# Performance work log

Hardware: AMD Instinct MI355X
Metric: run time of the kernel (lower is better)

Reference implementation:

```python
import jax, jax.numpy as jnp
import numpy as np

N_NODES = 20000
N_EDGES = 320000
N_GRAPHS = 64
IN_DIM = 768
HID = 256
HEADS = 4
NUM_CLASSES = 5
NEG_SLOPE = 0.2  # PyG GATConv default leaky_relu slope


def setup_inputs() -> dict:
    key = jax.random.key(0)
    ks = jax.random.split(key, 20)
    x = jax.random.normal(ks[0], (N_NODES, IN_DIM), dtype=jnp.float32)
    edge_index = jax.random.randint(ks[1], (2, N_EDGES), 0, N_NODES, dtype=jnp.int32)
    batch = jnp.sort(jax.random.randint(ks[2], (N_NODES,), 0, N_GRAPHS, dtype=jnp.int32))
    s = lambda k, sh: jax.random.normal(k, sh, dtype=jnp.float32) * (1.0 / np.sqrt(sh[0]))
    HC = HEADS * HID
    return {
        "x": x, "edge_index": edge_index, "batch": batch,
        "Wp": s(ks[3], (IN_DIM, HID)), "bp": jnp.zeros((HID,), jnp.float32),
        "W1": s(ks[4], (HID, HC)),
        "as1": jax.random.normal(ks[5], (HEADS, HID)) * 0.1,
        "ad1": jax.random.normal(ks[6], (HEADS, HID)) * 0.1,
        "b1": jnp.zeros((HC,), jnp.float32),
        "W2": s(ks[7], (HC, HC)),
        "as2": jax.random.normal(ks[8], (HEADS, HID)) * 0.1,
        "ad2": jax.random.normal(ks[9], (HEADS, HID)) * 0.1,
        "b2": jnp.zeros((HC,), jnp.float32),
        "Wc1": s(ks[10], (2 * HC, 256)), "bc1": jnp.zeros((256,), jnp.float32),
        "Wc2": s(ks[11], (256, NUM_CLASSES)), "bc2": jnp.zeros((NUM_CLASSES,), jnp.float32),
    }


def _gat(h, src, dst, W, att_s, att_d, bias):
    # PyG GATConv (concat=True), dropout in eval mode (identity).
    N = h.shape[0]
    hW = (h @ W).reshape(N, HEADS, HID)             # [N,H,C]
    a_s = jnp.einsum('nhc,hc->nh', hW, att_s)        # per-node src score
    a_d = jnp.einsum('nhc,hc->nh', hW, att_d)
    e = jax.nn.leaky_relu(a_s[src] + a_d[dst], NEG_SLOPE)  # [E,H]
    # segment softmax over incoming edges of each destination node
    m = jax.ops.segment_max(e, dst, num_segments=N)
    e = jnp.exp(e - m[dst])
    denom = jax.ops.segment_sum(e, dst, num_segments=N)
    alpha = e / (denom[dst] + 1e-16)
    msg = hW[src] * alpha[:, :, None]                # [E,H,C]
    out = jax.ops.segment_sum(msg, dst, num_segments=N)
    return out.reshape(N, HEADS * HID) + bias


def reference(x, edge_index, batch, Wp, bp, W1, as1, ad1, b1, W2, as2, ad2, b2, Wc1, bc1, Wc2, bc2):
    N = x.shape[0]
    # add self-loops (PyG GATConv default add_self_loops=True)
    loop = jnp.arange(N, dtype=edge_index.dtype)
    src = jnp.concatenate([edge_index[0], loop])
    dst = jnp.concatenate([edge_index[1], loop])

    h = jax.nn.relu(x @ Wp + bp)
    h = jax.nn.elu(_gat(h, src, dst, W1, as1, ad1, b1))
    h = jax.nn.elu(_gat(h, src, dst, W2, as2, ad2, b2))

    # global mean / max pool over graphs
    cnt = jax.ops.segment_sum(jnp.ones((N,), h.dtype), batch, num_segments=N_GRAPHS)
    mean_pool = jax.ops.segment_sum(h, batch, num_segments=N_GRAPHS) / jnp.maximum(cnt, 1.0)[:, None]
    max_pool = jax.ops.segment_max(h, batch, num_segments=N_GRAPHS)
    g = jnp.concatenate([mean_pool, max_pool], axis=1)  # [G, 2*H*C]

    hcls = jax.nn.relu(g @ Wc1 + bc1)
    return hcls @ Wc2 + bc2
```

## Files before the change

kernel.cpp:

```cpp
#include <hip/hip_runtime.h>
#include <hip/hip_fp16.h>
#include <math.h>

#define N_HID 256
#define N_HEADS 4
#define N_HC 1024
#define N_GRAPHS 64

typedef __attribute__((ext_vector_type(4))) float f32x4;
typedef _Float16 half8 __attribute__((ext_vector_type(8)));
typedef _Float16 half4 __attribute__((ext_vector_type(4)));

__device__ __forceinline__ void gl_lds16h(const __half* g, __half* l) {
    __builtin_amdgcn_global_load_lds(
        (const __attribute__((address_space(1))) unsigned int*)g,
        (__attribute__((address_space(3))) unsigned int*)l, 16, 0, 0);
}

__global__ __launch_bounds__(256) void k_deg(const int* __restrict__ dst, int E,
                                             int* __restrict__ deg) {
    int e = blockIdx.x * 256 + threadIdx.x;
    if (e < E) atomicAdd(&deg[dst[e]], 1);
}

__global__ __launch_bounds__(1024) void k_scan(const int* __restrict__ deg,
                                               int* __restrict__ rowstart, int N) {
    __shared__ int part[1024];
    const int t = threadIdx.x;
    const int chunk = (N + 1023) / 1024;
    const int c0 = t * chunk;
    int s = 0;
    for (int i = 0; i < chunk; i++) {
        int idx = c0 + i;
        if (idx < N) s += deg[idx];
    }
    part[t] = s;
    __syncthreads();
    for (int off = 1; off < 1024; off <<= 1) {
        int v = (t >= off) ? part[t - off] : 0;
        __syncthreads();
        part[t] += v;
        __syncthreads();
    }
    int run = (t == 0) ? 0 : part[t - 1];
    if (t == 0) rowstart[0] = 0;
    for (int i = 0; i < chunk; i++) {
        int idx = c0 + i;
        if (idx < N) {
            run += deg[idx];
            rowstart[idx + 1] = run;
        }
    }
}

__global__ __launch_bounds__(256) void k_fill(const int* __restrict__ src,
                                              const int* __restrict__ dst, int E,
                                              const int* __restrict__ rowstart,
                                              int* __restrict__ cursor,
                                              int* __restrict__ col) {
    int e = blockIdx.x * 256 + threadIdx.x;
    if (e < E) {
        int d = dst[e];
        int p = atomicAdd(&cursor[d], 1);
        col[rowstart[d] + p] = src[e];
    }
}

__global__ __launch_bounds__(256) void k_wtt(const float* __restrict__ W,
                                             __half* __restrict__ WT, int K, int N) {
    __shared__ float tile[32][33];
    const int k0 = blockIdx.y * 32, n0 = blockIdx.x * 32;
    const int tr = threadIdx.x >> 5, tc = threadIdx.x & 31;
#pragma unroll
    for (int rr = 0; rr < 4; rr++) {
        int k = k0 + tr + rr * 8;
        tile[tr + rr * 8][tc] = W[(size_t)k * N + n0 + tc];
    }
    __syncthreads();
#pragma unroll
    for (int rr = 0; rr < 4; rr++) {
        int n = n0 + tr + rr * 8;
        WT[(size_t)n * K + k0 + tc] = __float2half(tile[tc][tr + rr * 8]);
    }
}

__global__ __launch_bounds__(256) void k_makeva(const __half* __restrict__ W1T,
                                                const float* __restrict__ as1,
                                                const float* __restrict__ ad1,
                                                float* __restrict__ va) {
    __shared__ float satt[256];
    int b = blockIdx.x;
    int h = b & 3, isd = b >> 2;
    int k = threadIdx.x;
    const float* att = (isd ? ad1 : as1) + h * 256;
    satt[k] = att[k];
    __syncthreads();
    const __half* wr = W1T + (size_t)(h * 256) * 256 + k;
    float s = 0.f;
    for (int c = 0; c < 256; c++) s += __half2float(wr[(size_t)c * 256]) * satt[c];
    va[b * 256 + k] = s;
}

__global__ __launch_bounds__(256) void k_makeva2(const __half* __restrict__ W2T,
                                                 const float* __restrict__ as2,
                                                 const float* __restrict__ ad2,
                                                 float* __restrict__ va2) {
    __shared__ float satt[32];
    int b = blockIdx.x;
    int h = b & 3;
    int jc = blockIdx.y;
    int t = threadIdx.x;
    const float* att = (b >= 4 ? ad2 : as2) + h * 256 + jc * 32;
    if (t < 32) satt[t] = att[t];
    __syncthreads();
    float s0 = 0.f, s1 = 0.f, s2 = 0.f, s3 = 0.f;
    const __half* base = W2T + (size_t)(h * 256 + jc * 32) * 1024 + t * 4;
    for (int j = 0; j < 32; j++) {
        half4 wv = *reinterpret_cast<const half4*>(base + (size_t)j * 1024);
        float a = satt[j];
        s0 += a * (float)wv[0]; s1 += a * (float)wv[1];
        s2 += a * (float)wv[2]; s3 += a * (float)wv[3];
    }
    float* o = va2 + b * 1024 + t * 4;
    atomicAdd(o + 0, s0); atomicAdd(o + 1, s1);
    atomicAdd(o + 2, s2); atomicAdd(o + 3, s3);
}

template <int EPI, int COSCHED>
__global__ __launch_bounds__(256) void k_gemm2p(
    const __half* __restrict__ A, const __half* __restrict__ BT,
    const float* __restrict__ bias, __half* __restrict__ C,
    int M, int NROW, int K, int lda, int ldc,
    int aoffz, int boffz, int coffz, int bofz) {
    __shared__ __half sA[2][128 * 32];
    __shared__ __half sB[2][128 * 32];
    int bm, bn;
    size_t coff = 0;
    if (COSCHED) {
        const int bid = blockIdx.x;
        const int xcd = bid & 7, j0 = bid >> 3;
        const int br = xcd + 8 * (j0 >> 3);
        const int bc = j0 & 7;
        if (br >= NROW) return;
        bm = br * 128; bn = bc * 128;
    } else {
        const int z = blockIdx.z;
        A += (size_t)z * aoffz;
        BT += (size_t)z * boffz;
        bias += z * bofz;
        coff = (size_t)z * coffz;
        bm = blockIdx.y * 128; bn = blockIdx.x * 128;
    }
    const int tid = threadIdx.x, lane = tid & 63, w = tid >> 6;
    const int wr = (w >> 1) * 64, wc = (w & 1) * 64;
    const bool isB = (w >= 2);
    const __half* gsrc = isB ? (BT + (size_t)bn * K) : (A + (size_t)bm * lda);
    const int gld = isB ? K : lda;
    const int rbase = (w & 1) * 64;
    const int lr = lane >> 2, lsl = lane & 3;
    const int g = lane >> 4, fr = lane & 15;
    const int nt = K >> 5;

    f32x4 acc[4][4] = {};

    auto STAGE = [&](int b, int t) {
        __half* sbuf = (isB ? sB[b] : sA[b]);
        const int k0 = t << 5;
#pragma unroll
        for (int c2 = 0; c2 < 4; c2++) {
            int row = rbase + c2 * 16 + lr;
            int slg = lsl ^ ((row >> 1) & 3);
            gl_lds16h(gsrc + (size_t)row * gld + k0 + slg * 8,
                      sbuf + (rbase + c2 * 16) * 32);
        }
    };

    STAGE(0, 0);
    int cur = 0;
    for (int t = 0; t < nt; ++t) {
        if (t + 1 < nt) {
            STAGE(cur ^ 1, t + 1);
            asm volatile("s_waitcnt vmcnt(4)" ::: "memory");
        } else {
            asm volatile("s_waitcnt vmcnt(0)" ::: "memory");
        }
        asm volatile("s_barrier" ::: "memory");
        half8 af[4], bf[4];
#pragma unroll
        for (int i = 0; i < 4; i++) {
            int Ra = wr + i * 16 + fr;
            af[i] = *reinterpret_cast<const half8*>(
                &sA[cur][Ra * 32 + ((g ^ ((Ra >> 1) & 3)) << 3)]);
            int Rb = wc + i * 16 + fr;
            bf[i] = *reinterpret_cast<const half8*>(
                &sB[cur][Rb * 32 + ((g ^ ((Rb >> 1) & 3)) << 3)]);
        }
#pragma unroll
        for (int i = 0; i < 4; i++)
#pragma unroll
            for (int j = 0; j < 4; j++)
                acc[i][j] = __builtin_amdgcn_mfma_f32_16x16x32_f16(af[i], bf[j], acc[i][j], 0, 0, 0);
        asm volatile("s_barrier" ::: "memory");
        cur ^= 1;
    }
    const int crow0 = (lane >> 4) * 4, ccol = lane & 15;
#pragma unroll
    for (int i = 0; i < 4; i++)
#pragma unroll
        for (int j = 0; j < 4; j++) {
            int cc = bn + wc + j * 16 + ccol;
            float bv = (EPI == 2) ? bias[cc] : 0.f;
#pragma unroll
            for (int r = 0; r < 4; r++) {
                int row = bm + wr + i * 16 + crow0 + r;
                if (row < M) {
                    float v = acc[i][j][r];
                    if (EPI == 2) { v += bv; v = v > 0.f ? v : (__expf(v) - 1.f); }
                    C[(size_t)row * ldc + coff + cc] = __float2half(v);
                }
            }
        }
}

__global__ __launch_bounds__(256) void k_gemm_x(
    const float* __restrict__ A, const __half* __restrict__ BT,
    const float* __restrict__ bias, __half* __restrict__ C,
    int M, int NROW, int K, int lda) {
    __shared__ __half sA[128 * 32];
    __shared__ __half sB[128 * 32];
    const int bid = blockIdx.x;
    const int xcd = bid & 7, j0 = bid >> 3;
    const int br = xcd + 8 * (j0 >> 1);
    const int bc = j0 & 1;
    if (br >= NROW) return;
    const int bm = br * 128, bn = bc * 128;
    const int tid = threadIdx.x, lane = tid & 63, w = tid >> 6;
    const int wr = (w >> 1) * 64, wc = (w & 1) * 64;
    const int sm = tid >> 1, skb = (tid & 1) * 16;
    const bool rok = (bm + sm) < M;
    const int ph0 = (((tid & 1) * 2 + 0) ^ ((sm >> 1) & 3)) << 3;
    const int ph1 = (((tid & 1) * 2 + 1) ^ ((sm >> 1) & 3)) << 3;
    const int lr = lane >> 2, lsl = lane & 3;

    f32x4 acc[4][4] = {};

    for (int k0 = 0; k0 < K; k0 += 32) {
#pragma unroll
        for (int c = 0; c < 2; c++) {
            int rb = (w + c * 4) * 16;
            int row = rb + lr;
            int slg = lsl ^ ((row >> 1) & 3);
            gl_lds16h(BT + (size_t)(bn + row) * K + k0 + slg * 8, sB + rb * 32);
        }
        {
            const float* Arow = A + (size_t)(bm + sm) * lda + k0 + skb;
            float4 v0 = make_float4(0.f, 0.f, 0.f, 0.f), v1 = v0, v2 = v0, v3 = v0;
            if (rok) {
                v0 = *(const float4*)(Arow + 0);
                v1 = *(const float4*)(Arow + 4);
                v2 = *(const float4*)(Arow + 8);
                v3 = *(const float4*)(Arow + 12);
            }
            half8 ha, hb;
            ha[0] = (_Float16)v0.x; ha[1] = (_Float16)v0.y;
            ha[2] = (_Float16)v0.z; ha[3] = (_Float16)v0.w;
            ha[4] = (_Float16)v1.x; ha[5] = (_Float16)v1.y;
            ha[6] = (_Float16)v1.z; ha[7] = (_Float16)v1.w;
            hb[0] = (_Float16)v2.x; hb[1] = (_Float16)v2.y;
            hb[2] = (_Float16)v2.z; hb[3] = (_Float16)v2.w;
            hb[4] = (_Float16)v3.x; hb[5] = (_Float16)v3.y;
            hb[6] = (_Float16)v3.z; hb[7] = (_Float16)v3.w;
            *reinterpret_cast<half8*>(&sA[sm * 32 + ph0]) = ha;
            *reinterpret_cast<half8*>(&sA[sm * 32 + ph1]) = hb;
        }
        __syncthreads();
        half8 af[4], bf[4];
        const int g = lane >> 4, fr = lane & 15;
#pragma unroll
        for (int i = 0; i < 4; i++) {
            int Ra = wr + i * 16 + fr;
            af[i] = *reinterpret_cast<const half8*>(
                &sA[Ra * 32 + ((g ^ ((Ra >> 1) & 3)) << 3)]);
            int Rb = wc + i * 16 + fr;
            bf[i] = *reinterpret_cast<const half8*>(
                &sB[Rb * 32 + ((g ^ ((Rb >> 1) & 3)) << 3)]);
        }
#pragma unroll
        for (int i = 0; i < 4; i++)
#pragma unroll
            for (int j = 0; j < 4; j++)
                acc[i][j] = __builtin_amdgcn_mfma_f32_16x16x32_f16(af[i], bf[j], acc[i][j], 0, 0, 0);
        __syncthreads();
    }
    const int crow0 = (lane >> 4) * 4, ccol = lane & 15;
#pragma unroll
    for (int i = 0; i < 4; i++)
#pragma unroll
        for (int j = 0; j < 4; j++) {
            int cc = bn + wc + j * 16 + ccol;
            float bv = bias[cc];
#pragma unroll
            for (int r = 0; r < 4; r++) {
                int row = bm + wr + i * 16 + crow0 + r;
                if (row < M) {
                    float v = acc[i][j][r] + bv;
                    v = v > 0.f ? v : 0.f;
                    C[(size_t)row * 256 + cc] = __float2half(v);
                }
            }
        }
}

__global__ __launch_bounds__(256) void k_score8(const __half* __restrict__ h0,
                                                const float* __restrict__ va,
                                                float* __restrict__ a_s,
                                                float* __restrict__ a_d, int N) {
    __shared__ float sva[8][256];
    int t = threadIdx.x;
    for (int i = t; i < 2048; i += 256) sva[i >> 8][i & 255] = va[i];
    __syncthreads();
    int wv = t >> 6, lane = t & 63;
    int n = blockIdx.x * 4 + wv;
    if (n >= N) return;
    uint2 u = *(const uint2*)(h0 + (size_t)n * 256 + lane * 4);
    __half2 q0 = __builtin_bit_cast(__half2, u.x);
    __half2 q1 = __builtin_bit_cast(__half2, u.y);
    float v0 = __half2float(q0.x), v1 = __half2float(q0.y);
    float v2 = __half2float(q1.x), v3 = __half2float(q1.y);
    float p[8];
#pragma unroll
    for (int v = 0; v < 8; v++) {
        p[v] = v0 * sva[v][lane * 4] + v1 * sva[v][lane * 4 + 1] +
               v2 * sva[v][lane * 4 + 2] + v3 * sva[v][lane * 4 + 3];
    }
#pragma unroll
    for (int off = 32; off > 0; off >>= 1)
#pragma unroll
        for (int v = 0; v < 8; v++) p[v] += __shfl_xor(p[v], off, 64);
    if (lane == 0) {
        *(float4*)&a_s[n * 4] = make_float4(p[0], p[1], p[2], p[3]);
        *(float4*)&a_d[n * 4] = make_float4(p[4], p[5], p[6], p[7]);
    }
}

__global__ __launch_bounds__(256) void k_score1024(const __half* __restrict__ h1,
                                                   const float* __restrict__ va2,
                                                   float* __restrict__ a_s,
                                                   float* __restrict__ a_d, int N) {
    __shared__ float sva[8 * 1024];
    int t = threadIdx.x;
    for (int i = t; i < 8192; i += 256) sva[i] = va2[i];
    __syncthreads();
    int wv = t >> 6, lane = t & 63;
    int n = blockIdx.x * 4 + wv;
    if (n >= N) return;
    const __half* hp = h1 + (size_t)n * 1024;
    float hv[16];
#pragma unroll
    for (int seg = 0; seg < 4; seg++) {
        half4 u = *reinterpret_cast<const half4*>(hp + seg * 256 + lane * 4);
#pragma unroll
        for (int c = 0; c < 4; c++) hv[seg * 4 + c] = (float)u[c];
    }
    float p[8] = {};
#pragma unroll
    for (int v = 0; v < 8; v++) {
#pragma unroll
        for (int seg = 0; seg < 4; seg++) {
            float4 f = *(const float4*)&sva[v * 1024 + seg * 256 + lane * 4];
            p[v] += hv[seg * 4] * f.x + hv[seg * 4 + 1] * f.y +
                    hv[seg * 4 + 2] * f.z + hv[seg * 4 + 3] * f.w;
        }
    }
#pragma unroll
    for (int off = 32; off > 0; off >>= 1)
#pragma unroll
        for (int v = 0; v < 8; v++) p[v] += __shfl_xor(p[v], off, 64);
    if (lane == 0) {
        *(float4*)&a_s[n * 4] = make_float4(p[0], p[1], p[2], p[3]);
        *(float4*)&a_d[n * 4] = make_float4(p[4], p[5], p[6], p[7]);
    }
}

__global__ __launch_bounds__(256) void k_alpha(
    const float* __restrict__ a_s, const float* __restrict__ a_d,
    const int* __restrict__ rowstart, const int* __restrict__ col,
    __half* __restrict__ alp, float* __restrict__ invS, int N) {
    const int w = threadIdx.x >> 6, lane = threadIdx.x & 63;
    const int n = blockIdx.x * 4 + w;
    if (n >= N) return;
    const int e0 = rowstart[n];
    const int deg = rowstart[n + 1] - e0;
    const int tot = deg + 1;
    const int as0 = e0 + n;
    float4 adv4 = *(const float4*)&a_d[n * 4];
    const float adv[4] = {adv4.x, adv4.y, adv4.z, adv4.w};
    float M[4] = {-INFINITY, -INFINITY, -INFINITY, -INFINITY};
    for (int base = 0; base < tot; base += 64) {
        const int li = base + lane;
        float e[4] = {-INFINITY, -INFINITY, -INFINITY, -INFINITY};
        if (li < tot) {
            const int sn = (li < deg) ? col[e0 + li] : n;
            float4 asv = *(const float4*)&a_s[sn * 4];
            const float as4[4] = {asv.x, asv.y, asv.z, asv.w};
#pragma unroll
            for (int h = 0; h < 4; h++) {
                float sc = as4[h] + adv[h];
                e[h] = sc >= 0.f ? sc : 0.2f * sc;
            }
        }
#pragma unroll
        for (int off = 32; off > 0; off >>= 1)
#pragma unroll
            for (int h = 0; h < 4; h++)
                e[h] = fmaxf(e[h], __shfl_xor(e[h], off, 64));
#pragma unroll
        for (int h = 0; h < 4; h++) M[h] = fmaxf(M[h], e[h]);
    }
    float S[4] = {0.f, 0.f, 0.f, 0.f};
    for (int base = 0; base < tot; base += 64) {
        const int li = base + lane;
        float wv[4] = {0.f, 0.f, 0.f, 0.f};
        if (li < tot) {
            const int sn = (li < deg) ? col[e0 + li] : n;
            float4 asv = *(const float4*)&a_s[sn * 4];
            const float as4[4] = {asv.x, asv.y, asv.z, asv.w};
            half4 o;
#pragma unroll
            for (int h = 0; h < 4; h++) {
                float sc = as4[h] + adv[h];
                float e = sc >= 0.f ? sc : 0.2f * sc;
                wv[h] = __expf(e - M[h]);
                o[h] = (_Float16)wv[h];
            }
            *reinterpret_cast<half4*>(alp + (size_t)(as0 + li) * 4) = o;
        }
        float sw[4] = {wv[0], wv[1], wv[2], wv[3]};
#pragma unroll
        for (int off = 32; off > 0; off >>= 1)
#pragma unroll
            for (int h = 0; h < 4; h++) sw[h] += __shfl_xor(sw[h], off, 64);
#pragma unroll
        for (int h = 0; h < 4; h++) S[h] += sw[h];
    }
    if (lane == 0) {
        *(float4*)&invS[n * 4] = make_float4(
            1.f / (S[0] + 1e-16f), 1.f / (S[1] + 1e-16f),
            1.f / (S[2] + 1e-16f), 1.f / (S[3] + 1e-16f));
    }
}

__global__ __launch_bounds__(256) void k_gath1(
    const __half* __restrict__ h0, const __half* __restrict__ alp,
    const float* __restrict__ invS, const int* __restrict__ rowstart,
    const int* __restrict__ col, __half* __restrict__ agg1, int N) {
    __shared__ int wsn[4][64];
    __shared__ float wal[4][64][4];
    const int w = threadIdx.x >> 6, lane = threadIdx.x & 63;
    const int bid = blockIdx.x;
    const int s = bid & 1;
    const int n = (bid >> 1) * 4 + w;
    if (n >= N) return;
    const int e0 = rowstart[n];
    const int deg = rowstart[n + 1] - e0;
    const int tot = deg + 1;
    const int as0 = e0 + n;
    float acc[4][2] = {};

    for (int base = 0; base < tot; base += 64) {
        const int cnt = min(64, tot - base);
        const int li = base + lane;
        if (li < tot) {
            wsn[w][lane] = (li < deg) ? col[e0 + li] : n;
            half4 av = *reinterpret_cast<const half4*>(alp + (size_t)(as0 + li) * 4);
            *(float4*)&wal[w][lane][0] = make_float4(
                (float)av[0], (float)av[1], (float)av[2], (float)av[3]);
        }
        const __half* gbase = h0 + s * 128 + lane * 2;
#pragma unroll 2
        for (int i = 0; i < cnt; i++) {
            const int s2 = wsn[w][i];
            float4 wg = *(const float4*)&wal[w][i][0];
            const float wgt[4] = {wg.x, wg.y, wg.z, wg.w};
            __half2 hv = *(const __half2*)(gbase + (size_t)s2 * 256);
            float v0 = __half2float(hv.x), v1 = __half2float(hv.y);
#pragma unroll
            for (int h = 0; h < 4; h++) {
                acc[h][0] += wgt[h] * v0;
                acc[h][1] += wgt[h] * v1;
            }
        }
    }
    float4 dv = *(const float4*)&invS[n * 4];
    const float d[4] = {dv.x, dv.y, dv.z, dv.w};
#pragma unroll
    for (int h = 0; h < 4; h++) {
        __half2 o;
        o.x = __float2half(acc[h][0] * d[h]);
        o.y = __float2half(acc[h][1] * d[h]);
        *(__half2*)(agg1 + (size_t)n * 1024 + h * 256 + s * 128 + lane * 2) = o;
    }
}

__global__ __launch_bounds__(256) void k_gath2(
    const __half* __restrict__ hW, const __half* __restrict__ alp,
    const float* __restrict__ invS, const int* __restrict__ rowstart,
    const int* __restrict__ col, const float* __restrict__ bias,
    __half* __restrict__ h2, int N) {
    __shared__ int wsn[4][64];
    __shared__ float wal[4][64];
    const int w = threadIdx.x >> 6, lane = threadIdx.x & 63;
    const int bid = blockIdx.x;
    const int h = bid & 3;
    const int n = (bid >> 2) * 4 + w;
    if (n >= N) return;
    const int e0 = rowstart[n];
    const int deg = rowstart[n + 1] - e0;
    const int tot = deg + 1;
    const int as0 = e0 + n;
    float acc[4] = {};

    for (int base = 0; base < tot; base += 64) {
        const int cnt = min(64, tot - base);
        const int li = base + lane;
        if (li < tot) {
            wsn[w][lane] = (li < deg) ? col[e0 + li] : n;
            wal[w][lane] = (float)alp[(size_t)(as0 + li) * 4 + h];
        }
        const __half* gbase = hW + h * 256 + lane * 4;
#pragma unroll 4
        for (int i = 0; i < cnt; i++) {
            const int s2 = wsn[w][i];
            const float a = wal[w][i];
            half4 v = *reinterpret_cast<const half4*>(gbase + (size_t)s2 * 1024);
#pragma unroll
            for (int c = 0; c < 4; c++) acc[c] += a * (float)v[c];
        }
    }
    const float d = invS[n * 4 + h];
    const int cc = h * 256 + lane * 4;
    float4 bb = *(const float4*)&bias[cc];
    const float bv[4] = {bb.x, bb.y, bb.z, bb.w};
    half4 o;
#pragma unroll
    for (int c = 0; c < 4; c++) {
        float v = acc[c] * d + bv[c];
        v = v > 0.f ? v : (__expf(v) - 1.f);
        o[c] = (_Float16)v;
    }
    *reinterpret_cast<half4*>(h2 + (size_t)n * 1024 + cc) = o;
}

__global__ __launch_bounds__(128) void k_gbounds(const int* __restrict__ batch, int N,
                                                 int* __restrict__ gstart) {
    int g = threadIdx.x;
    if (g > N_GRAPHS) return;
    if (g == N_GRAPHS) { gstart[N_GRAPHS] = N; return; }
    int lo = 0, hi = N;
    while (lo < hi) {
        int mid = (lo + hi) >> 1;
        if (batch[mid] < g) lo = mid + 1; else hi = mid;
    }
    gstart[g] = lo;
}

__global__ __launch_bounds__(256) void k_pool1(const __half* __restrict__ h,
                                               const int* __restrict__ gstart,
                                               float* __restrict__ ps) {
    const int g = blockIdx.x, c = blockIdx.y, t = threadIdx.x;
    const int s = gstart[g], e = gstart[g + 1];
    const int len = e - s;
    const int cs = s + (int)(((long long)len * c) >> 3);
    const int ce = s + (int)(((long long)len * (c + 1)) >> 3);
    float sum[4] = {};
    float mx[4] = {-INFINITY, -INFINITY, -INFINITY, -INFINITY};
    for (int i = cs; i < ce; i++) {
        half4 v = *reinterpret_cast<const half4*>(h + (size_t)i * N_HC + t * 4);
#pragma unroll
        for (int k = 0; k < 4; k++) {
            float f = (float)v[k];
            sum[k] += f;
            mx[k] = fmaxf(mx[k], f);
        }
    }
    float* o = ps + ((size_t)g * 8 + c) * 2048;
    *(float4*)&o[t * 4] = make_float4(sum[0], sum[1], sum[2], sum[3]);
    *(float4*)&o[1024 + t * 4] = make_float4(mx[0], mx[1], mx[2], mx[3]);
}

__global__ __launch_bounds__(256) void k_pool2(const float* __restrict__ ps,
                                               const int* __restrict__ gstart,
                                               float* __restrict__ gout) {
    const int g = blockIdx.x, t = threadIdx.x;
    float sum[4] = {};
    float mx[4] = {-INFINITY, -INFINITY, -INFINITY, -INFINITY};
#pragma unroll
    for (int c = 0; c < 8; c++) {
        const float* o = ps + ((size_t)g * 8 + c) * 2048;
        float4 sv = *(const float4*)&o[t * 4];
        float4 mv = *(const float4*)&o[1024 + t * 4];
        sum[0] += sv.x; sum[1] += sv.y; sum[2] += sv.z; sum[3] += sv.w;
        mx[0] = fmaxf(mx[0], mv.x); mx[1] = fmaxf(mx[1], mv.y);
        mx[2] = fmaxf(mx[2], mv.z); mx[3] = fmaxf(mx[3], mv.w);
    }
    float cnt = fmaxf((float)(gstart[g + 1] - gstart[g]), 1.f);
    float inv = 1.f / cnt;
    *(float4*)(gout + (size_t)g * 2048 + t * 4) =
        make_float4(sum[0] * inv, sum[1] * inv, sum[2] * inv, sum[3] * inv);
    *(float4*)(gout + (size_t)g * 2048 + 1024 + t * 4) =
        make_float4(mx[0], mx[1], mx[2], mx[3]);
}

__global__ __launch_bounds__(256) void k_cls1p(const float* __restrict__ g,
                                               const float* __restrict__ Wc1,
                                               float* __restrict__ hacc) {
    __shared__ float gs[256];
    const int gb = blockIdx.x, kc = blockIdx.y, t = threadIdx.x;
    gs[t] = g[(size_t)gb * 2048 + kc * 256 + t];
    __syncthreads();
    float acc = 0.f;
    const float* wb = Wc1 + (size_t)(kc * 256) * 256 + t;
#pragma unroll 4
    for (int k = 0; k < 256; k++) acc += gs[k] * wb[(size_t)k * 256];
    atomicAdd(&hacc[gb * 256 + t], acc);
}

__global__ __launch_bounds__(256) void k_cls2(const float* __restrict__ hacc,
                                              const float* __restrict__ bc1,
                                              const float* __restrict__ Wc2,
                                              const float* __restrict__ bc2,
                                              float* __restrict__ out) {
    int idx = blockIdx.x * 256 + threadIdx.x;
    if (idx >= N_GRAPHS * 5) return;
    int gb = idx / 5, j = idx % 5;
    float acc = 0.f;
    for (int k = 0; k < 256; k++) {
        float v = hacc[gb * 256 + k] + bc1[k];
        v = v > 0.f ? v : 0.f;
        acc += v * Wc2[k * 5 + j];
    }
    out[idx] = acc + bc2[j];
}

extern "C" void kernel_launch(void* const* d_in, const int* in_sizes, int n_in,
                              void* d_out, int out_size, void* d_ws, size_t ws_size,
                              hipStream_t stream) {
    const float* x    = (const float*)d_in[0];
    const int*   ei   = (const int*)d_in[1];
    const int*   batch= (const int*)d_in[2];
    const float* Wp   = (const float*)d_in[3];
    const float* bp   = (const float*)d_in[4];
    const float* W1   = (const float*)d_in[5];
    const float* as1  = (const float*)d_in[6];
    const float* ad1  = (const float*)d_in[7];
    const float* b1   = (const float*)d_in[8];
    const float* W2   = (const float*)d_in[9];
    const float* as2  = (const float*)d_in[10];
    const float* ad2  = (const float*)d_in[11];
    const float* b2   = (const float*)d_in[12];
    const float* Wc1  = (const float*)d_in[13];
    const float* bc1  = (const float*)d_in[14];
    const float* Wc2  = (const float*)d_in[15];
    const float* bc2  = (const float*)d_in[16];
    float* out = (float*)d_out;

    const int N = in_sizes[0] / 768;
    const int E = in_sizes[1] / 2;
    const int MP = ((N + 127) / 128) * 128;
    const int MB = MP / 128;

    const int* src = ei;
    const int* dst = ei + E;

    char* ws = (char*)d_ws;
    size_t off = 0;
    auto give = [&](size_t bytes) -> void* {
        void* p = ws + off;
        off = (off + bytes + 255) & ~(size_t)255;
        return p;
    };
    __half* h0  = (__half*)give((size_t)MP * N_HID * 2);
    __half* agg1= (__half*)give((size_t)MP * N_HC * 2);
    __half* h1  = (__half*)give((size_t)MP * N_HC * 2);
    __half* hW2 = (__half*)give((size_t)MP * N_HC * 2);
    __half* h2  = (__half*)give((size_t)MP * N_HC * 2);
    __half* WpT = (__half*)give((size_t)768 * 256 * 2);
    __half* W1T = (__half*)give((size_t)256 * 1024 * 2);
    __half* W2T = (__half*)give((size_t)1024 * 1024 * 2);
    float* va   = (float*)give((size_t)8 * 256 * 4);
    float* va2  = (float*)give((size_t)8 * 1024 * 4);
    float* a_s1 = (float*)give((size_t)N * N_HEADS * 4);
    float* a_d1 = (float*)give((size_t)N * N_HEADS * 4);
    float* a_s2 = (float*)give((size_t)N * N_HEADS * 4);
    float* a_d2 = (float*)give((size_t)N * N_HEADS * 4);
    __half* alp1 = (__half*)give((size_t)(E + N) * 4 * 2);
    __half* alp2 = (__half*)give((size_t)(E + N) * 4 * 2);
    float* invS1 = (float*)give((size_t)N * 4 * 4);
    float* invS2 = (float*)give((size_t)N * 4 * 4);
    float* ps   = (float*)give((size_t)N_GRAPHS * 8 * 2048 * 4);
    int* deg     = (int*)give((size_t)N * 4);
    int* cursor  = (int*)give((size_t)N * 4);
    int* rowstart= (int*)give((size_t)(N + 1) * 4);
    int* col     = (int*)give((size_t)E * 4);
    int* gstart  = (int*)give((size_t)(N_GRAPHS + 1) * 4);
    float* gpool = (float*)give((size_t)N_GRAPHS * 2048 * 4);
    float* hacc  = (float*)give((size_t)N_GRAPHS * 256 * 4);
    (void)ws_size; (void)n_in; (void)out_size;

    hipMemsetAsync(deg, 0, (size_t)N * 4, stream);
    hipMemsetAsync(cursor, 0, (size_t)N * 4, stream);
    hipMemsetAsync(va2, 0, (size_t)8 * 1024 * 4, stream);
    hipMemsetAsync(hacc, 0, (size_t)N_GRAPHS * 256 * 4, stream);
    k_deg<<<(E + 255) / 256, 256, 0, stream>>>(dst, E, deg);
    k_scan<<<1, 1024, 0, stream>>>(deg, rowstart, N);
    k_fill<<<(E + 255) / 256, 256, 0, stream>>>(src, dst, E, rowstart, cursor, col);
    k_gbounds<<<1, 128, 0, stream>>>(batch, N, gstart);

    k_wtt<<<dim3(256 / 32, 768 / 32), 256, 0, stream>>>(Wp, WpT, 768, 256);
    k_wtt<<<dim3(1024 / 32, 256 / 32), 256, 0, stream>>>(W1, W1T, 256, 1024);
    k_wtt<<<dim3(1024 / 32, 1024 / 32), 256, 0, stream>>>(W2, W2T, 1024, 1024);
    k_makeva<<<8, 256, 0, stream>>>(W1T, as1, ad1, va);
    k_makeva2<<<dim3(8, 8), 256, 0, stream>>>(W2T, as2, ad2, va2);

    const int NROWPAD = ((MB + 7) / 8) * 8;
    const int NGB = (N + 3) / 4;

    k_gemm_x<<<NROWPAD * 2, 256, 0, stream>>>(x, WpT, bp, h0, N, MB, 768, 768);

    k_score8<<<NGB, 256, 0, stream>>>(h0, va, a_s1, a_d1, N);
    k_alpha<<<NGB, 256, 0, stream>>>(a_s1, a_d1, rowstart, col, alp1, invS1, N);
    k_gath1<<<NGB * 2, 256, 0, stream>>>(h0, alp1, invS1, rowstart, col, agg1, N);
    k_gemm2p<2, 0><<<dim3(2, MB, 4), 256, 0, stream>>>(
        agg1, W1T, b1, h1, N, 0, 256, 1024, 1024, 256, 65536, 256, 256);

    k_score1024<<<NGB, 256, 0, stream>>>(h1, va2, a_s2, a_d2, N);
    k_alpha<<<NGB, 256, 0, stream>>>(a_s2, a_d2, rowstart, col, alp2, invS2, N);
    k_gemm2p<0, 1><<<NROWPAD * 8, 256, 0, stream>>>(
        h1, W2T, nullptr, hW2, N, MB, 1024, 1024, 1024, 0, 0, 0, 0);
    k_gath2<<<NGB * 4, 256, 0, stream>>>(
        hW2, alp2, invS2, rowstart, col, b2, h2, N);

    k_pool1<<<dim3(N_GRAPHS, 8), 256, 0, stream>>>(h2, gstart, ps);
    k_pool2<<<N_GRAPHS, 256, 0, stream>>>(ps, gstart, gpool);
    k_cls1p<<<dim3(N_GRAPHS, 8), 256, 0, stream>>>(gpool, Wc1, hacc);
    k_cls2<<<2, 256, 0, stream>>>(hacc, bc1, Wc2, bc2, out);
}
```

Baseline: 445.9 us.

## Fuse layer-1 attention softmax into gather and triple-buffer GEMM LDS pipeline

Removes the separate k_alpha pass for layer 1 and computes edge scores, an online softmax (running max and sum with rescaling) and the weighted aggregation inside k_gath1. Each wave now covers all 256 channels of a node with 4 channels per lane, instead of splitting the channels across two blocks. This avoids writing and re-reading alp1/invS1 and one kernel launch, at the cost of more registers and fewer blocks. Separately, the k_gemm2p K-loop moves from double to triple buffering with a two-stage prefetch, which increases LDS use per block.

```diff
diff --git a/kernel.cpp b/kernel.cpp
--- a/kernel.cpp
+++ b/kernel.cpp
@@ -132,8 +132,8 @@
     const float* __restrict__ bias, __half* __restrict__ C,
     int M, int NROW, int K, int lda, int ldc,
     int aoffz, int boffz, int coffz, int bofz) {
-    __shared__ __half sA[2][128 * 32];
-    __shared__ __half sB[2][128 * 32];
+    __shared__ __half sA[3][128 * 32];
+    __shared__ __half sB[3][128 * 32];
     int bm, bn;
     size_t coff = 0;
     if (COSCHED) {
@@ -176,10 +176,13 @@
     };
 
     STAGE(0, 0);
-    int cur = 0;
+    if (nt > 1) STAGE(1, 1);
     for (int t = 0; t < nt; ++t) {
-        if (t + 1 < nt) {
-            STAGE(cur ^ 1, t + 1);
+        const int cur = t % 3;
+        if (t + 2 < nt) {
+            STAGE((t + 2) % 3, t + 2);
+            asm volatile("s_waitcnt vmcnt(8)" ::: "memory");
+        } else if (t + 1 < nt) {
             asm volatile("s_waitcnt vmcnt(4)" ::: "memory");
         } else {
             asm volatile("s_waitcnt vmcnt(0)" ::: "memory");
@@ -201,7 +204,6 @@
             for (int j = 0; j < 4; j++)
                 acc[i][j] = __builtin_amdgcn_mfma_f32_16x16x32_f16(af[i], bf[j], acc[i][j], 0, 0, 0);
         asm volatile("s_barrier" ::: "memory");
-        cur ^= 1;
     }
     const int crow0 = (lane >> 4) * 4, ccol = lane & 15;
 #pragma unroll
@@ -451,54 +453,87 @@
 }
 
 __global__ __launch_bounds__(256) void k_gath1(
-    const __half* __restrict__ h0, const __half* __restrict__ alp,
-    const float* __restrict__ invS, const int* __restrict__ rowstart,
+    const __half* __restrict__ h0, const float* __restrict__ a_s,
+    const float* __restrict__ a_d, const int* __restrict__ rowstart,
     const int* __restrict__ col, __half* __restrict__ agg1, int N) {
     __shared__ int wsn[4][64];
     __shared__ float wal[4][64][4];
     const int w = threadIdx.x >> 6, lane = threadIdx.x & 63;
-    const int bid = blockIdx.x;
-    const int s = bid & 1;
-    const int n = (bid >> 1) * 4 + w;
+    const int n = blockIdx.x * 4 + w;
     if (n >= N) return;
     const int e0 = rowstart[n];
     const int deg = rowstart[n + 1] - e0;
     const int tot = deg + 1;
-    const int as0 = e0 + n;
-    float acc[4][2] = {};
+    float4 adv4 = *(const float4*)&a_d[n * 4];
+    const float adv[4] = {adv4.x, adv4.y, adv4.z, adv4.w};
+    float M[4] = {-INFINITY, -INFINITY, -INFINITY, -INFINITY};
+    float S[4] = {0.f, 0.f, 0.f, 0.f};
+    float acc[4][4] = {};
 
     for (int base = 0; base < tot; base += 64) {
         const int cnt = min(64, tot - base);
-        const int li = base + lane;
-        if (li < tot) {
-            wsn[w][lane] = (li < deg) ? col[e0 + li] : n;
-            half4 av = *reinterpret_cast<const half4*>(alp + (size_t)(as0 + li) * 4);
-            *(float4*)&wal[w][lane][0] = make_float4(
-                (float)av[0], (float)av[1], (float)av[2], (float)av[3]);
-        }
-        const __half* gbase = h0 + s * 128 + lane * 2;
+        const bool act = lane < cnt;
+        int sn = n;
+        float e[4] = {-INFINITY, -INFINITY, -INFINITY, -INFINITY};
+        if (act) {
+            const int li = base + lane;
+            sn = (li < deg) ? col[e0 + li] : n;
+            float4 asv = *(const float4*)&a_s[sn * 4];
+            const float as4[4] = {asv.x, asv.y, asv.z, asv.w};
+#pragma unroll
+            for (int h = 0; h < 4; h++) {
+                float sc = as4[h] + adv[h];
+                e[h] = sc >= 0.f ? sc : 0.2f * sc;
+            }
+        }
+        float mw[4] = {e[0], e[1], e[2], e[3]};
+#pragma unroll
+        for (int off = 32; off > 0; off >>= 1)
+#pragma unroll
+            for (int h = 0; h < 4; h++)
+                mw[h] = fmaxf(mw[h], __shfl_xor(mw[h], off, 64));
+        float wv[4], sw[4];
+#pragma unroll
+        for (int h = 0; h < 4; h++) {
+            mw[h] = fmaxf(mw[h], M[h]);
+            wv[h] = act ? __expf(e[h] - mw[h]) : 0.f;
+            sw[h] = wv[h];
+        }
+        wsn[w][lane] = sn;
+        *(float4*)&wal[w][lane][0] = make_float4(wv[0], wv[1], wv[2], wv[3]);
+#pragma unroll
+        for (int off = 32; off > 0; off >>= 1)
+#pragma unroll
+            for (int h = 0; h < 4; h++) sw[h] += __shfl_xor(sw[h], off, 64);
+#pragma unroll
+        for (int h = 0; h < 4; h++) {
+            float sc = __expf(M[h] - mw[h]);
+            S[h] = S[h] * sc + sw[h];
+#pragma unroll
+            for (int c = 0; c < 4; c++) acc[h][c] *= sc;
+            M[h] = mw[h];
+        }
+        const __half* gbase = h0 + lane * 4;
 #pragma unroll 2
         for (int i = 0; i < cnt; i++) {
             const int s2 = wsn[w][i];
             float4 wg = *(const float4*)&wal[w][i][0];
             const float wgt[4] = {wg.x, wg.y, wg.z, wg.w};
-            __half2 hv = *(const __half2*)(gbase + (size_t)s2 * 256);
-            float v0 = __half2float(hv.x), v1 = __half2float(hv.y);
-#pragma unroll
-            for (int h = 0; h < 4; h++) {
-                acc[h][0] += wgt[h] * v0;
-                acc[h][1] += wgt[h] * v1;
-            }
-        }
-    }
-    float4 dv = *(const float4*)&invS[n * 4];
-    const float d[4] = {dv.x, dv.y, dv.z, dv.w};
+            half4 v = *reinterpret_cast<const half4*>(gbase + (size_t)s2 * 256);
+            const float vf[4] = {(float)v[0], (float)v[1], (float)v[2], (float)v[3]};
+#pragma unroll
+            for (int h = 0; h < 4; h++)
+#pragma unroll
+                for (int c = 0; c < 4; c++) acc[h][c] += wgt[h] * vf[c];
+        }
+    }
 #pragma unroll
     for (int h = 0; h < 4; h++) {
-        __half2 o;
-        o.x = __float2half(acc[h][0] * d[h]);
-        o.y = __float2half(acc[h][1] * d[h]);
-        *(__half2*)(agg1 + (size_t)n * 1024 + h * 256 + s * 128 + lane * 2) = o;
+        float d = 1.f / (S[h] + 1e-16f);
+        half4 o;
+#pragma unroll
+        for (int c = 0; c < 4; c++) o[c] = (_Float16)(acc[h][c] * d);
+        *reinterpret_cast<half4*>(agg1 + (size_t)n * 1024 + h * 256 + lane * 4) = o;
     }
 }
 
@@ -693,9 +728,7 @@
     float* a_d1 = (float*)give((size_t)N * N_HEADS * 4);
     float* a_s2 = (float*)give((size_t)N * N_HEADS * 4);
     float* a_d2 = (float*)give((size_t)N * N_HEADS * 4);
-    __half* alp1 = (__half*)give((size_t)(E + N) * 4 * 2);
     __half* alp2 = (__half*)give((size_t)(E + N) * 4 * 2);
-    float* invS1 = (float*)give((size_t)N * 4 * 4);
     float* invS2 = (float*)give((size_t)N * 4 * 4);
     float* ps   = (float*)give((size_t)N_GRAPHS * 8 * 2048 * 4);
     int* deg     = (int*)give((size_t)N * 4);
@@ -728,8 +761,7 @@
     k_gemm_x<<<NROWPAD * 2, 256, 0, stream>>>(x, WpT, bp, h0, N, MB, 768, 768);
 
     k_score8<<<NGB, 256, 0, stream>>>(h0, va, a_s1, a_d1, N);
-    k_alpha<<<NGB, 256, 0, stream>>>(a_s1, a_d1, rowstart, col, alp1, invS1, N);
-    k_gath1<<<NGB * 2, 256, 0, stream>>>(h0, alp1, invS1, rowstart, col, agg1, N);
+    k_gath1<<<NGB, 256, 0, stream>>>(h0, a_s1, a_d1, rowstart, col, agg1, N);
     k_gemm2p<2, 0><<<dim3(2, MB, 4), 256, 0, stream>>>(
         agg1, W1T, b1, h1, N, 0, 256, 1024, 1024, 256, 65536, 256, 256);
 
```

Result: no change. 452.8 us (+1.6%).
